# Performance work log

Hardware: AMD Instinct MI355X
Metric: run time of the kernel (lower is better)

## Reference

```python
import jax, jax.numpy as jnp
import jax.scipy.linalg as jsp
import numpy as np

# Problem dimensions (match init_kwargs P_shape/A_shape)
N = 256   # variables
M = 512   # constraints
B = 64    # batch

# OSQP ADMM hyper-parameters (fixed-rho variant of the OSQP algorithm)
SIGMA = 1e-6
RHO = 0.1
ALPHA = 1.6
N_ITERS = 500


def setup_inputs() -> dict:
    key = jax.random.key(0)
    kP, kq, kA, kc = jax.random.split(key, 4)
    # P is diagonal with strictly positive entries -> PSD (values are the nnz of P)
    P_val = jax.random.uniform(kP, (B, N), dtype=jnp.float32) + 0.1
    q_val = jax.random.normal(kq, (B, N), dtype=jnp.float32)
    # A is a dense pattern; values stored row-major as its nnz vector
    A_val = jax.random.normal(kA, (B, M * N), dtype=jnp.float32) / np.sqrt(N)
    # Feasible box: l <= u by construction
    center = jax.random.normal(kc, (B, M), dtype=jnp.float32)
    l_val = center - 1.0
    u_val = center + 1.0
    return {"P_val": P_val, "q_val": q_val, "A_val": A_val, "l_val": l_val, "u_val": u_val}


def _admm_qp(P_val, q_val, A_val, l_val, u_val):
    """Batched OSQP-style ADMM solve of min 1/2 x'Px + q'x  s.t. l <= Ax <= u.

    P is diagonal (nnz pattern = diag), A is dense (nnz pattern = full m x n).
    """
    A = A_val.reshape(B, M, N)                      # [B,m,n]
    # KKT-like matrix M_k = P + sigma*I + rho*A'A   [B,n,n]
    eye = jnp.eye(N, dtype=P_val.dtype)
    P_diag = P_val + SIGMA                          # diagonal of P + sigma*I
    Mk = RHO * jnp.einsum('bmi,bmj->bij', A, A) + jax.vmap(jnp.diag)(P_diag)
    L = jnp.linalg.cholesky(Mk)                     # [B,n,n], factor once, reuse
    Lt = jnp.swapaxes(L, -1, -2)

    def kkt_solve(rhs):                             # rhs [B,n]
        y1 = jsp.solve_triangular(L, rhs[..., None], lower=True)
        y2 = jsp.solve_triangular(Lt, y1, lower=False)
        return y2[..., 0]

    x0 = jnp.zeros((B, N), dtype=P_val.dtype)
    z0 = jnp.zeros((B, M), dtype=P_val.dtype)
    y0 = jnp.zeros((B, M), dtype=P_val.dtype)

    def step(state, _):
        x, z, y = state
        rhs = SIGMA * x - q_val + jnp.einsum('bmn,bm->bn', A, RHO * z - y)
        x_t = kkt_solve(rhs)                        # x-tilde
        z_t = jnp.einsum('bmn,bn->bm', A, x_t)      # z-tilde = A x_t
        x_new = ALPHA * x_t + (1.0 - ALPHA) * x
        z_hat = ALPHA * z_t + (1.0 - ALPHA) * z
        z_new = jnp.clip(z_hat + y / RHO, l_val, u_val)
        y_new = y + RHO * (z_hat - z_new)
        return (x_new, z_new, y_new), None

    (x, _, _), _ = jax.lax.scan(step, (x0, z0, y0), None, length=N_ITERS)
    return x


def reference(P_val, q_val, A_val, l_val, u_val):
    return _admm_qp(P_val, q_val, A_val, l_val, u_val)   # [B, n] primal solutions
```

## Files before the change

kernel.cpp:

```cpp
#include <hip/hip_runtime.h>
#include <hip/hip_fp16.h>

#define N_VAR 256
#define M_CON 512
#define BATCH 64
#define SIGMA_C 1e-6f
#define RHO_C 0.1f
#define ALPHA_C 1.6f
#define NITERS 500

__global__ __launch_bounds__(256) void k_transpose(const float* __restrict__ A,
                                                   float* __restrict__ At) {
  __shared__ float tile[32][33];
  int b = blockIdx.z;
  int n0 = blockIdx.x * 32;
  int m0 = blockIdx.y * 32;
  const float* Ab = A + (size_t)b * (M_CON * N_VAR);
  float* Atb = At + (size_t)b * (M_CON * N_VAR);
  int tx = threadIdx.x, ty = threadIdx.y;
#pragma unroll
  for (int j = 0; j < 32; j += 8)
    tile[ty + j][tx] = Ab[(size_t)(m0 + ty + j) * N_VAR + n0 + tx];
  __syncthreads();
#pragma unroll
  for (int j = 0; j < 32; j += 8)
    Atb[(size_t)(n0 + ty + j) * M_CON + m0 + tx] = tile[tx][ty + j];
}

__global__ __launch_bounds__(256) void k_ntgemm(
    const float* __restrict__ X, const float* __restrict__ Y,
    float* __restrict__ C, int I, int J, int K,
    long long bsX, long long bsY, long long bsC, float alpha,
    const float* __restrict__ diagv, int tilesJ, int packC) {
  int b = blockIdx.y;
  int ti = blockIdx.x / tilesJ, tj = blockIdx.x % tilesJ;
  int i0 = ti * 128, j0 = tj * 128;
  const float* Xb = X + (size_t)b * bsX;
  const float* Yb = Y + (size_t)b * bsY;
  float* Cb = C + (size_t)b * bsC;
  __shared__ float Xs[16][128];
  __shared__ float Ys[16][128];
  int tid = threadIdx.x;
  int tx = tid & 15, ty = tid >> 4;
  float acc[8][8];
#pragma unroll
  for (int r = 0; r < 8; ++r)
#pragma unroll
    for (int c = 0; c < 8; ++c) acc[r][c] = 0.0f;

  for (int kk = 0; kk < K; kk += 16) {
#pragma unroll
    for (int v = 0; v < 2; ++v) {
      int idx = v * 256 + tid;
      int row = idx >> 2;
      int k4 = (idx & 3) * 4;
      float4 gx = *(const float4*)(Xb + (size_t)(i0 + row) * K + kk + k4);
      Xs[k4 + 0][row] = gx.x; Xs[k4 + 1][row] = gx.y;
      Xs[k4 + 2][row] = gx.z; Xs[k4 + 3][row] = gx.w;
      float4 gy = *(const float4*)(Yb + (size_t)(j0 + row) * K + kk + k4);
      Ys[k4 + 0][row] = gy.x; Ys[k4 + 1][row] = gy.y;
      Ys[k4 + 2][row] = gy.z; Ys[k4 + 3][row] = gy.w;
    }
    __syncthreads();
#pragma unroll
    for (int k = 0; k < 16; ++k) {
      float xr[8], yr[8];
      *(float4*)&xr[0] = *(float4*)&Xs[k][ty * 8];
      *(float4*)&xr[4] = *(float4*)&Xs[k][ty * 8 + 4];
      *(float4*)&yr[0] = *(float4*)&Ys[k][tx * 8];
      *(float4*)&yr[4] = *(float4*)&Ys[k][tx * 8 + 4];
#pragma unroll
      for (int r = 0; r < 8; ++r)
#pragma unroll
        for (int c = 0; c < 8; ++c) acc[r][c] += xr[r] * yr[c];
    }
    __syncthreads();
  }
  if (packC) {
    unsigned* Cp = (unsigned*)Cb;
#pragma unroll
    for (int r = 0; r < 8; ++r) {
      int gi = i0 + ty * 8 + r;
      int sl = gi >> 7, rl = gi & 127;
      int rh = rl >> 6, ll = rl & 63;
#pragma unroll
      for (int c = 0; c < 8; c += 2) {
        int gj = j0 + tx * 8 + c;
        int cg = gj >> 7, j2 = (gj & 127) >> 1;
        int t2 = ((((cg << 1) | rh) << 6) | ll);
        __half2 hh = __floats2half2_rn(acc[r][c] * alpha, acc[r][c + 1] * alpha);
        Cp[(size_t)sl * 32768 + j2 * 512 + t2] = *(unsigned*)&hh;
      }
    }
    return;
  }
#pragma unroll
  for (int r = 0; r < 8; ++r) {
    int gi = i0 + ty * 8 + r;
#pragma unroll
    for (int c = 0; c < 8; ++c) {
      int gj = j0 + tx * 8 + c;
      float val = acc[r][c] * alpha;
      if (diagv != nullptr && gi == gj) val += diagv[(size_t)b * N_VAR + gi] + SIGMA_C;
      Cb[(size_t)gi * J + gj] = val;
    }
  }
}

__global__ __launch_bounds__(512, 2) void k_invert(const float* __restrict__ Mk,
                                                   float* __restrict__ Mi) {
  int b = blockIdx.x;
  const float* src = Mk + (size_t)b * 65536;
  float* dst = Mi + (size_t)b * 65536;
  int t = threadIdx.x;
  int c = t & 255, rh = t >> 8;

  float a[128];
#pragma unroll
  for (int j = 0; j < 128; ++j) a[j] = src[(size_t)(rh * 128 + j) * 256 + c];

  __shared__ float colPan[256][8];
  __shared__ float rowPan[2][8][260];
  __shared__ float PiSh[64];
  __shared__ float Rp[8][260];

  int rh_s = __builtin_amdgcn_readfirstlane(rh);
  int cw_s = __builtin_amdgcn_readfirstlane((t >> 6) & 3);

  if (rh == 0) {
#pragma unroll
    for (int j = 0; j < 8; ++j) rowPan[0][j][c] = a[j];
  }
  __syncthreads();

  for (int s = 0; s < 32; ++s) {
    int kb = s * 8;
    int cur = s & 1, nxt = cur ^ 1;
    int kh = kb >> 7, kj = kb & 127;
    int khn = (kb + 8) >> 7, kjn = (kb + 8) & 127;
    bool mycol = (c >= kb) && (c < kb + 8);

    if (cw_s == (kb >> 6)) {
      if (mycol) {
        int f = c - kb;
#pragma unroll
        for (int j = 0; j < 128; ++j) colPan[rh * 128 + j][f] = a[j];
      }
    }
    if (t < 64) {
      int e = t >> 3, f = t & 7;
      float p = rowPan[cur][e][kb + f];
#pragma unroll
      for (int k2 = 0; k2 < 8; ++k2) {
        float piv = __shfl(p, k2 * 8 + k2);
        float rv = __shfl(p, k2 * 8 + f);
        float cv = __shfl(p, e * 8 + k2);
        float pivinv = 1.0f / piv;
        float srv = rv * pivinv;
        float gen = p - cv * srv;
        p = gen;
        if (e == k2) p = srv;
        if (f == k2) p = -cv * pivinv;
        if (e == k2 && f == k2) p = pivinv;
      }
      PiSh[t] = p;
    }
    __syncthreads();

    float rpan[8];
#pragma unroll
    for (int f2 = 0; f2 < 8; ++f2) rpan[f2] = rowPan[cur][f2][c];
    float rp[8];
#pragma unroll
    for (int e = 0; e < 8; ++e) {
      float4 p0 = *(const float4*)&PiSh[e * 8];
      float4 p1 = *(const float4*)&PiSh[e * 8 + 4];
      rp[e] = p0.x * rpan[0] + p0.y * rpan[1] + p0.z * rpan[2] + p0.w * rpan[3] +
              p1.x * rpan[4] + p1.y * rpan[5] + p1.z * rpan[6] + p1.w * rpan[7];
    }
    if (cw_s == (kb >> 6)) {
      if (mycol) {
        int f = c - kb;
#pragma unroll
        for (int e = 0; e < 8; ++e) rp[e] = PiSh[e * 8 + f];
      }
    }
#pragma unroll
    for (int e = 0; e < 8; ++e) Rp[e][c] = rp[e];

    bool myhalfk = (rh_s == kh);
    bool stashw = (s != 31) && (rh_s == khn);
#pragma unroll
    for (int j = 0; j < 128; ++j) {
      float4 c0 = *(const float4*)&colPan[rh * 128 + j][0];
      float4 c1 = *(const float4*)&colPan[rh * 128 + j][4];
      float aold = a[j];
      float nv = aold -
                 (c0.x * rp[0] + c0.y * rp[1] + c0.z * rp[2] + c0.w * rp[3] +
                  c1.x * rp[4] + c1.y * rp[5] + c1.z * rp[6] + c1.w * rp[7]);
      if (mycol) nv -= aold;
      if (myhalfk && j >= kj && j < kj + 8)
        nv = Rp[j - kj][c];
      a[j] = nv;
      if (stashw && j >= kjn && j < kjn + 8)
        rowPan[nxt][j - kjn][c] = nv;
    }
    __syncthreads();
  }

#pragma unroll
  for (int j = 0; j < 128; ++j) dst[(size_t)(rh * 128 + j) * 256 + c] = a[j];
}

__global__ __launch_bounds__(256) void k_matvec_h(const float* __restrict__ Mi,
                                                  const float* __restrict__ q,
                                                  float* __restrict__ h) {
  int b = blockIdx.x, t = threadIdx.x;
  __shared__ float qs[256];
  qs[t] = q[(size_t)b * 256 + t];
  __syncthreads();
  const float* Mb = Mi + (size_t)b * 65536;
  float acc = 0.0f;
  for (int k = 0; k < 256; ++k) acc += Mb[(size_t)k * 256 + t] * qs[k];
  h[(size_t)b * 256 + t] = acc;
}

__global__ __launch_bounds__(512) void k_matvec_d(const float* __restrict__ At,
                                                  const float* __restrict__ h,
                                                  float* __restrict__ d) {
  int b = blockIdx.x, t = threadIdx.x;
  __shared__ float hs[256];
  if (t < 256) hs[t] = h[(size_t)b * 256 + t];
  __syncthreads();
  const float* Ab = At + (size_t)b * 131072;
  float acc = 0.0f;
  for (int n = 0; n < 256; ++n) acc += Ab[(size_t)n * 512 + t] * hs[n];
  d[(size_t)b * 512 + t] = acc;
}

__global__ __launch_bounds__(512) void k_admm4(
    const unsigned* __restrict__ Gpk_g, const float* __restrict__ dvec,
    const float* __restrict__ lv, const float* __restrict__ uv,
    unsigned long long* __restrict__ wtag, float* __restrict__ Sbuf) {
  int g = blockIdx.x;
  int b = (g & 7) + 8 * ((g >> 3) & 7);
  int s = g >> 6;
  int t = threadIdx.x;
  int l = t & 63, wv = t >> 6;
  int c0 = wv * 64;
  int cg = wv >> 1, hc = wv & 1;

  __shared__ __align__(16) float wbuf[8][64];
  __shared__ float part[2][8][128];

  const unsigned* gsrc =
      Gpk_g + (size_t)(b * 4 + s) * 32768 + (size_t)(hc * 32) * 512 + cg * 128 + l;

  float zreg = 0.0f, yreg = 0.0f, Sreg = 0.0f;
  float lreg = 0.0f, ureg = 0.0f, dreg = 0.0f;
  if (t < 128) {
    lreg = lv[(size_t)b * 512 + s * 128 + t];
    ureg = uv[(size_t)b * 512 + s * 128 + t];
    dreg = dvec[(size_t)b * 512 + s * 128 + t];
  }
  wbuf[wv][l] = 0.0f;

  unsigned long long* wt0 = wtag + (size_t)b * 512;
  unsigned long long* wt1 = wtag + 32768 + (size_t)b * 512;
  const float4* wq4 = (const float4*)(wbuf[wv]);

  for (int it = 0; it < NITERS; ++it) {
    if (it > 0) {
      unsigned long long* wp = (it & 1) ? wt1 : wt0;
      unsigned want = (unsigned)it;
      unsigned long long v = __hip_atomic_load(&wp[c0 + l], __ATOMIC_RELAXED,
                                               __HIP_MEMORY_SCOPE_AGENT);
      bool got = ((unsigned)(v >> 32) == want);
      while (!__all(got)) {
        if (!got) {
          unsigned long long v2 = __hip_atomic_load(
              &wp[c0 + l], __ATOMIC_RELAXED, __HIP_MEMORY_SCOPE_AGENT);
          if ((unsigned)(v2 >> 32) == want) { v = v2; got = true; }
        }
      }
      wbuf[wv][l] = __uint_as_float((unsigned)(v & 0xffffffffu));
    }

    float r0a = 0.f, r0b = 0.f, r1a = 0.f, r1b = 0.f;
#pragma unroll
    for (int j = 0; j < 8; ++j) {
      float4 wa = wq4[2 * j];
      float4 wc = wq4[2 * j + 1];
      unsigned a0 = gsrc[(4 * j + 0) * 512];
      unsigned a1 = gsrc[(4 * j + 1) * 512];
      unsigned a2 = gsrc[(4 * j + 2) * 512];
      unsigned a3 = gsrc[(4 * j + 3) * 512];
      unsigned b0 = gsrc[(4 * j + 0) * 512 + 64];
      unsigned b1 = gsrc[(4 * j + 1) * 512 + 64];
      unsigned b2 = gsrc[(4 * j + 2) * 512 + 64];
      unsigned b3 = gsrc[(4 * j + 3) * 512 + 64];
      float2 fa0 = __half22float2(*(__half2*)&a0);
      float2 fa1 = __half22float2(*(__half2*)&a1);
      float2 fa2 = __half22float2(*(__half2*)&a2);
      float2 fa3 = __half22float2(*(__half2*)&a3);
      float2 fb0 = __half22float2(*(__half2*)&b0);
      float2 fb1 = __half22float2(*(__half2*)&b1);
      float2 fb2 = __half22float2(*(__half2*)&b2);
      float2 fb3 = __half22float2(*(__half2*)&b3);
      r0a += fa0.x * wa.x + fa0.y * wa.y + fa1.x * wa.z + fa1.y * wa.w;
      r0b += fa2.x * wc.x + fa2.y * wc.y + fa3.x * wc.z + fa3.y * wc.w;
      r1a += fb0.x * wa.x + fb0.y * wa.y + fb1.x * wa.z + fb1.y * wa.w;
      r1b += fb2.x * wc.x + fb2.y * wc.y + fb3.x * wc.z + fb3.y * wc.w;
    }
    int pp = it & 1;
    part[pp][wv][l] = r0a + r0b;
    part[pp][wv][64 + l] = r1a + r1b;
    __syncthreads();

    if (t < 128) {
      float w_old = RHO_C * zreg - yreg;
      Sreg = w_old - 0.6f * Sreg;
      float p = part[pp][0][t] + part[pp][1][t] + part[pp][2][t] +
                part[pp][3][t] + part[pp][4][t] + part[pp][5][t] +
                part[pp][6][t] + part[pp][7][t];
      float zt = p - dreg;
      float zh = ALPHA_C * zt + (1.0f - ALPHA_C) * zreg;
      float zc = zh + yreg * (1.0f / RHO_C);
      zc = fminf(fmaxf(zc, lreg), ureg);
      yreg += RHO_C * (zh - zc);
      zreg = zc;
      if (it < NITERS - 1) {
        float wn = RHO_C * zreg - yreg;
        unsigned long long pk =
            ((unsigned long long)(unsigned)(it + 1) << 32) |
            (unsigned long long)__float_as_uint(wn);
        unsigned long long* wp = ((it + 1) & 1) ? wt1 : wt0;
        __hip_atomic_store(&wp[s * 128 + t], pk, __ATOMIC_RELAXED,
                           __HIP_MEMORY_SCOPE_AGENT);
      }
    }
  }

  if (t < 128) Sbuf[(size_t)b * 512 + s * 128 + t] = Sreg;
}

__global__ __launch_bounds__(256) void k_final(
    const float* __restrict__ A, const float* __restrict__ q,
    const float* __restrict__ Mi, const float* __restrict__ Sbuf,
    float* __restrict__ xout) {
  int b = blockIdx.x, t = threadIdx.x;
  __shared__ float Ssh[512];
  __shared__ float uu[256];
  for (int i = t; i < 512; i += 256) Ssh[i] = Sbuf[(size_t)b * 512 + i];
  __syncthreads();
  const float* Ab = A + (size_t)b * 131072;
  float acc = 0.0f;
  for (int m = 0; m < 512; ++m) acc += Ab[(size_t)m * 256 + t] * Ssh[m];
  uu[t] = ALPHA_C * acc - q[(size_t)b * 256 + t];
  __syncthreads();
  const float* Mb = Mi + (size_t)b * 65536;
  float x = 0.0f;
  for (int kk = 0; kk < 256; ++kk) x += Mb[(size_t)kk * 256 + t] * uu[kk];
  xout[(size_t)b * 256 + t] = x;
}

extern "C" void kernel_launch(void* const* d_in, const int* in_sizes, int n_in,
                              void* d_out, int out_size, void* d_ws, size_t ws_size,
                              hipStream_t stream) {
  (void)in_sizes; (void)n_in; (void)out_size; (void)ws_size;
  const float* P = (const float*)d_in[0];
  const float* q = (const float*)d_in[1];
  const float* Av = (const float*)d_in[2];
  const float* lv = (const float*)d_in[3];
  const float* uv = (const float*)d_in[4];
  float* xout = (float*)d_out;

  float* ws = (float*)d_ws;
  float* At = ws;
  float* F  = ws;
  float* Mi = ws + 8388608;
  float* Mk = ws + 12582912;
  float* Gp = ws + 12582912;
  float* hv = ws + 29360128;
  float* dv = ws + 29376512;
  float* Sbuf = ws + 29409280;
  unsigned long long* wtag = (unsigned long long*)ws;

  k_transpose<<<dim3(8, 16, 64), dim3(32, 8), 0, stream>>>(Av, At);
  k_ntgemm<<<dim3(4, 64), 256, 0, stream>>>(At, At, Mk, 256, 256, 512,
                                            131072LL, 131072LL, 65536LL,
                                            RHO_C, P, 2, 0);
  k_invert<<<64, 512, 0, stream>>>(Mk, Mi);
  k_matvec_h<<<64, 256, 0, stream>>>(Mi, q, hv);
  k_matvec_d<<<64, 512, 0, stream>>>(At, hv, dv);
  k_ntgemm<<<dim3(8, 64), 256, 0, stream>>>(Av, Mi, F, 512, 256, 256,
                                            131072LL, 65536LL, 131072LL,
                                            1.0f, nullptr, 2, 0);
  k_ntgemm<<<dim3(16, 64), 256, 0, stream>>>(F, Av, Gp, 512, 512, 256,
                                             131072LL, 131072LL, 131072LL,
                                             1.0f, nullptr, 4, 1);
  k_admm4<<<256, 512, 0, stream>>>((const unsigned*)Gp, dv, lv, uv, wtag, Sbuf);
  k_final<<<64, 256, 0, stream>>>(Av, q, Mi, Sbuf, xout);
}
```

Measured before the change: 1.541 ms.

## Keep G block resident in registers and double ADMM block threads

The persistent ADMM kernel now launches 1024 threads per block. Each thread preloads its 32 packed half2 entries of the G submatrix into registers once, instead of re-reading them from global memory on every iteration. The per-iteration matvec then runs from registers against the shared w vector, with each wave handling one row half for one column group. The risk is register pressure under launch_bounds(1024,4), which could cause spills, and a larger block that may make the per-iteration barrier and cross-block spin synchronisation more expensive.

```diff
diff --git a/kernel.cpp b/kernel.cpp
--- a/kernel.cpp
+++ b/kernel.cpp
@@ -238,7 +238,7 @@
   d[(size_t)b * 512 + t] = acc;
 }
 
-__global__ __launch_bounds__(512) void k_admm4(
+__global__ __launch_bounds__(1024, 4) void k_admm4(
     const unsigned* __restrict__ Gpk_g, const float* __restrict__ dvec,
     const float* __restrict__ lv, const float* __restrict__ uv,
     unsigned long long* __restrict__ wtag, float* __restrict__ Sbuf) {
@@ -247,15 +247,20 @@
   int s = g >> 6;
   int t = threadIdx.x;
   int l = t & 63, wv = t >> 6;
-  int c0 = wv * 64;
-  int cg = wv >> 1, hc = wv & 1;
-
-  __shared__ __align__(16) float wbuf[8][64];
+  int cg = wv & 7, rh = wv >> 3;
+  int c0 = cg * 64;
+
+  __shared__ __align__(16) float wbuf[16][64];
   __shared__ float part[2][8][128];
 
-  const unsigned* gsrc =
-      Gpk_g + (size_t)(b * 4 + s) * 32768 + (size_t)(hc * 32) * 512 + cg * 128 + l;
-
+  const unsigned* gsrc = Gpk_g + (size_t)(b * 4 + s) * 32768 +
+                         (size_t)((cg & 1) * 32) * 512 + (cg >> 1) * 128 +
+                         rh * 64 + l;
+  unsigned Gw[32];
+#pragma unroll
+  for (int k = 0; k < 32; ++k) Gw[k] = gsrc[(size_t)k * 512];
+
+  int row_local = rh * 64 + l;
   float zreg = 0.0f, yreg = 0.0f, Sreg = 0.0f;
   float lreg = 0.0f, ureg = 0.0f, dreg = 0.0f;
   if (t < 128) {
@@ -267,7 +272,7 @@
 
   unsigned long long* wt0 = wtag + (size_t)b * 512;
   unsigned long long* wt1 = wtag + 32768 + (size_t)b * 512;
-  const float4* wq4 = (const float4*)(wbuf[wv]);
+  const float* wrow = wbuf[wv];
 
   for (int it = 0; it < NITERS; ++it) {
     if (it > 0) {
@@ -286,35 +291,26 @@
       wbuf[wv][l] = __uint_as_float((unsigned)(v & 0xffffffffu));
     }
 
-    float r0a = 0.f, r0b = 0.f, r1a = 0.f, r1b = 0.f;
-#pragma unroll
-    for (int j = 0; j < 8; ++j) {
-      float4 wa = wq4[2 * j];
-      float4 wc = wq4[2 * j + 1];
-      unsigned a0 = gsrc[(4 * j + 0) * 512];
-      unsigned a1 = gsrc[(4 * j + 1) * 512];
-      unsigned a2 = gsrc[(4 * j + 2) * 512];
-      unsigned a3 = gsrc[(4 * j + 3) * 512];
-      unsigned b0 = gsrc[(4 * j + 0) * 512 + 64];
-      unsigned b1 = gsrc[(4 * j + 1) * 512 + 64];
-      unsigned b2 = gsrc[(4 * j + 2) * 512 + 64];
-      unsigned b3 = gsrc[(4 * j + 3) * 512 + 64];
-      float2 fa0 = __half22float2(*(__half2*)&a0);
-      float2 fa1 = __half22float2(*(__half2*)&a1);
-      float2 fa2 = __half22float2(*(__half2*)&a2);
-      float2 fa3 = __half22float2(*(__half2*)&a3);
-      float2 fb0 = __half22float2(*(__half2*)&b0);
-      float2 fb1 = __half22float2(*(__half2*)&b1);
-      float2 fb2 = __half22float2(*(__half2*)&b2);
-      float2 fb3 = __half22float2(*(__half2*)&b3);
-      r0a += fa0.x * wa.x + fa0.y * wa.y + fa1.x * wa.z + fa1.y * wa.w;
-      r0b += fa2.x * wc.x + fa2.y * wc.y + fa3.x * wc.z + fa3.y * wc.w;
-      r1a += fb0.x * wa.x + fb0.y * wa.y + fb1.x * wa.z + fb1.y * wa.w;
-      r1b += fb2.x * wc.x + fb2.y * wc.y + fb3.x * wc.z + fb3.y * wc.w;
+    float a0 = 0.f, a1 = 0.f, a2 = 0.f, a3 = 0.f;
+#pragma unroll
+    for (int k = 0; k < 32; k += 4) {
+      float4 w0 = *(const float4*)&wrow[2 * k];
+      float4 w1 = *(const float4*)&wrow[2 * k + 4];
+      __half2 h0 = *(__half2*)&Gw[k];
+      __half2 h1 = *(__half2*)&Gw[k + 1];
+      __half2 h2 = *(__half2*)&Gw[k + 2];
+      __half2 h3 = *(__half2*)&Gw[k + 3];
+      a0 = fmaf(__half2float(__low2half(h0)), w0.x, a0);
+      a1 = fmaf(__half2float(__high2half(h0)), w0.y, a1);
+      a2 = fmaf(__half2float(__low2half(h1)), w0.z, a2);
+      a3 = fmaf(__half2float(__high2half(h1)), w0.w, a3);
+      a0 = fmaf(__half2float(__low2half(h2)), w1.x, a0);
+      a1 = fmaf(__half2float(__high2half(h2)), w1.y, a1);
+      a2 = fmaf(__half2float(__low2half(h3)), w1.z, a2);
+      a3 = fmaf(__half2float(__high2half(h3)), w1.w, a3);
     }
     int pp = it & 1;
-    part[pp][wv][l] = r0a + r0b;
-    part[pp][wv][64 + l] = r1a + r1b;
+    part[pp][cg][row_local] = (a0 + a1) + (a2 + a3);
     __syncthreads();
 
     if (t < 128) {
@@ -399,6 +395,6 @@
   k_ntgemm<<<dim3(16, 64), 256, 0, stream>>>(F, Av, Gp, 512, 512, 256,
                                              131072LL, 131072LL, 131072LL,
                                              1.0f, nullptr, 4, 1);
-  k_admm4<<<256, 512, 0, stream>>>((const unsigned*)Gp, dv, lv, uv, wtag, Sbuf);
+  k_admm4<<<256, 1024, 0, stream>>>((const unsigned*)Gp, dv, lv, uv, wtag, Sbuf);
   k_final<<<64, 256, 0, stream>>>(Av, q, Mi, Sbuf, xout);
 }
```

After: 1.673 ms. +8.5%, slower.

## Compute G = F·Aᵀ with split-fp16 MFMA and prefetch G loads in ADMM loop

Applied to the files above, without the earlier changes.

Replaces the fp32 SIMT GEMM that builds the packed G matrix with an MFMA kernel. Each fp32 operand is split into a high fp16 part plus a scaled fp16 residual, and three MFMA products recover near-fp32 accuracy. A cast-split kernel is added for A, and the F GEMM now writes hi/lo fp16 halves directly. The ADMM loop now loads all G values for an iteration into registers before the spin-wait, so the loads overlap the synchronisation. wtag moves to its own region with an explicit memset. The cost is extra passes and workspace, higher register pressure in k_admm4, and some precision risk from the fp16 split.

```diff
diff --git a/kernel.cpp b/kernel.cpp
--- a/kernel.cpp
+++ b/kernel.cpp
@@ -8,6 +8,9 @@
 #define RHO_C 0.1f
 #define ALPHA_C 1.6f
 #define NITERS 500
+
+typedef _Float16 f16x8 __attribute__((ext_vector_type(8)));
+typedef float f32x4 __attribute__((ext_vector_type(4)));
 
 __global__ __launch_bounds__(256) void k_transpose(const float* __restrict__ A,
                                                    float* __restrict__ At) {
@@ -29,7 +32,7 @@
 
 __global__ __launch_bounds__(256) void k_ntgemm(
     const float* __restrict__ X, const float* __restrict__ Y,
-    float* __restrict__ C, int I, int J, int K,
+    float* __restrict__ C, float* __restrict__ C2, int I, int J, int K,
     long long bsX, long long bsY, long long bsC, float alpha,
     const float* __restrict__ diagv, int tilesJ, int packC) {
   int b = blockIdx.y;
@@ -37,7 +40,6 @@
   int i0 = ti * 128, j0 = tj * 128;
   const float* Xb = X + (size_t)b * bsX;
   const float* Yb = Y + (size_t)b * bsY;
-  float* Cb = C + (size_t)b * bsC;
   __shared__ float Xs[16][128];
   __shared__ float Ys[16][128];
   int tid = threadIdx.x;
@@ -76,24 +78,28 @@
     }
     __syncthreads();
   }
-  if (packC) {
-    unsigned* Cp = (unsigned*)Cb;
+  if (packC == 2) {
+    unsigned* Ch = (unsigned*)C + (size_t)b * 65536;
+    unsigned* Ce = (unsigned*)C2 + (size_t)b * 65536;
 #pragma unroll
     for (int r = 0; r < 8; ++r) {
       int gi = i0 + ty * 8 + r;
-      int sl = gi >> 7, rl = gi & 127;
-      int rh = rl >> 6, ll = rl & 63;
 #pragma unroll
       for (int c = 0; c < 8; c += 2) {
         int gj = j0 + tx * 8 + c;
-        int cg = gj >> 7, j2 = (gj & 127) >> 1;
-        int t2 = ((((cg << 1) | rh) << 6) | ll);
-        __half2 hh = __floats2half2_rn(acc[r][c] * alpha, acc[r][c + 1] * alpha);
-        Cp[(size_t)sl * 32768 + j2 * 512 + t2] = *(unsigned*)&hh;
+        float v0 = acc[r][c] * alpha, v1 = acc[r][c + 1] * alpha;
+        __half2 hh = __floats2half2_rn(v0, v1);
+        float2 fb = __half22float2(hh);
+        __half2 he = __floats2half2_rn((v0 - fb.x) * 256.0f,
+                                       (v1 - fb.y) * 256.0f);
+        int idx = gi * 128 + (gj >> 1);
+        Ch[idx] = *(unsigned*)&hh;
+        Ce[idx] = *(unsigned*)&he;
       }
     }
     return;
   }
+  float* Cb = C + (size_t)b * bsC;
 #pragma unroll
   for (int r = 0; r < 8; ++r) {
     int gi = i0 + ty * 8 + r;
@@ -105,6 +111,90 @@
       Cb[(size_t)gi * J + gj] = val;
     }
   }
+}
+
+__global__ __launch_bounds__(256) void k_cast_split(
+    const float* __restrict__ in, unsigned* __restrict__ oh,
+    unsigned* __restrict__ oe, int n4) {
+  int i = blockIdx.x * 256 + threadIdx.x;
+  if (i >= n4) return;
+  float4 v = ((const float4*)in)[i];
+  __half2 h01 = __floats2half2_rn(v.x, v.y);
+  __half2 h23 = __floats2half2_rn(v.z, v.w);
+  float2 f01 = __half22float2(h01);
+  float2 f23 = __half22float2(h23);
+  __half2 e01 = __floats2half2_rn((v.x - f01.x) * 256.0f, (v.y - f01.y) * 256.0f);
+  __half2 e23 = __floats2half2_rn((v.z - f23.x) * 256.0f, (v.w - f23.y) * 256.0f);
+  uint2 uh; uh.x = *(unsigned*)&h01; uh.y = *(unsigned*)&h23;
+  uint2 ue; ue.x = *(unsigned*)&e01; ue.y = *(unsigned*)&e23;
+  ((uint2*)oh)[i] = uh;
+  ((uint2*)oe)[i] = ue;
+}
+
+__global__ __launch_bounds__(256, 4) void k_mfma_g(
+    const _Float16* __restrict__ Fh, const _Float16* __restrict__ Fe,
+    const _Float16* __restrict__ Ah, const _Float16* __restrict__ Ae,
+    unsigned* __restrict__ Gp) {
+  int b = blockIdx.y;
+  int bx = blockIdx.x;
+  int t = threadIdx.x, l = t & 63, wv = t >> 6;
+  int i0 = (bx >> 2) * 32;
+  int j0 = (bx & 3) * 128 + wv * 32;
+  const _Float16* Fhb = Fh + (size_t)b * 131072;
+  const _Float16* Feb = Fe + (size_t)b * 131072;
+  const _Float16* Ahb = Ah + (size_t)b * 131072;
+  const _Float16* Aeb = Ae + (size_t)b * 131072;
+  unsigned* Gpb = Gp + (size_t)b * 131072;
+
+  int lr = l & 15, lk = (l >> 4) * 8;
+  f32x4 acc00 = {0,0,0,0}, acc01 = {0,0,0,0}, acc10 = {0,0,0,0}, acc11 = {0,0,0,0};
+  f32x4 ar00 = {0,0,0,0}, ar01 = {0,0,0,0}, ar10 = {0,0,0,0}, ar11 = {0,0,0,0};
+
+  for (int kk = 0; kk < 256; kk += 32) {
+    f16x8 af0 = *(const f16x8*)&Fhb[(size_t)(i0 + lr) * 256 + kk + lk];
+    f16x8 af1 = *(const f16x8*)&Fhb[(size_t)(i0 + 16 + lr) * 256 + kk + lk];
+    f16x8 ae0 = *(const f16x8*)&Feb[(size_t)(i0 + lr) * 256 + kk + lk];
+    f16x8 ae1 = *(const f16x8*)&Feb[(size_t)(i0 + 16 + lr) * 256 + kk + lk];
+    f16x8 bf0 = *(const f16x8*)&Ahb[(size_t)(j0 + lr) * 256 + kk + lk];
+    f16x8 bf1 = *(const f16x8*)&Ahb[(size_t)(j0 + 16 + lr) * 256 + kk + lk];
+    f16x8 be0 = *(const f16x8*)&Aeb[(size_t)(j0 + lr) * 256 + kk + lk];
+    f16x8 be1 = *(const f16x8*)&Aeb[(size_t)(j0 + 16 + lr) * 256 + kk + lk];
+    acc00 = __builtin_amdgcn_mfma_f32_16x16x32_f16(af0, bf0, acc00, 0, 0, 0);
+    acc01 = __builtin_amdgcn_mfma_f32_16x16x32_f16(af0, bf1, acc01, 0, 0, 0);
+    acc10 = __builtin_amdgcn_mfma_f32_16x16x32_f16(af1, bf0, acc10, 0, 0, 0);
+    acc11 = __builtin_amdgcn_mfma_f32_16x16x32_f16(af1, bf1, acc11, 0, 0, 0);
+    ar00 = __builtin_amdgcn_mfma_f32_16x16x32_f16(af0, be0, ar00, 0, 0, 0);
+    ar01 = __builtin_amdgcn_mfma_f32_16x16x32_f16(af0, be1, ar01, 0, 0, 0);
+    ar10 = __builtin_amdgcn_mfma_f32_16x16x32_f16(af1, be0, ar10, 0, 0, 0);
+    ar11 = __builtin_amdgcn_mfma_f32_16x16x32_f16(af1, be1, ar11, 0, 0, 0);
+    ar00 = __builtin_amdgcn_mfma_f32_16x16x32_f16(ae0, bf0, ar00, 0, 0, 0);
+    ar01 = __builtin_amdgcn_mfma_f32_16x16x32_f16(ae0, bf1, ar01, 0, 0, 0);
+    ar10 = __builtin_amdgcn_mfma_f32_16x16x32_f16(ae1, bf0, ar10, 0, 0, 0);
+    ar11 = __builtin_amdgcn_mfma_f32_16x16x32_f16(ae1, bf1, ar11, 0, 0, 0);
+  }
+
+#pragma unroll
+  for (int tr = 0; tr < 2; ++tr)
+#pragma unroll
+    for (int tc = 0; tc < 2; ++tc) {
+      const f32x4* am = (tr == 0) ? ((tc == 0) ? &acc00 : &acc01)
+                                  : ((tc == 0) ? &acc10 : &acc11);
+      const f32x4* ae = (tr == 0) ? ((tc == 0) ? &ar00 : &ar01)
+                                  : ((tc == 0) ? &ar10 : &ar11);
+#pragma unroll
+      for (int r = 0; r < 4; ++r) {
+        float v = (*am)[r] + (*ae)[r] * (1.0f / 256.0f);
+        float vp = __shfl_xor(v, 1);
+        int gi = i0 + tr * 16 + (l >> 4) * 4 + r;
+        int gj = j0 + tc * 16 + lr;
+        if (!(l & 1)) {
+          __half2 hh = __floats2half2_rn(v, vp);
+          int sl = gi >> 7, rl = gi & 127;
+          int t2 = ((((gj >> 7) << 1) | (rl >> 6)) << 6) | (rl & 63);
+          Gpb[(size_t)sl * 32768 + ((gj & 127) >> 1) * 512 + t2] = *(unsigned*)&hh;
+        }
+      }
+    }
 }
 
 __global__ __launch_bounds__(512, 2) void k_invert(const float* __restrict__ Mk,
@@ -270,6 +360,13 @@
   const float4* wq4 = (const float4*)(wbuf[wv]);
 
   for (int it = 0; it < NITERS; ++it) {
+    unsigned gva[32], gvb[32];
+#pragma unroll
+    for (int k = 0; k < 32; ++k) {
+      gva[k] = gsrc[(size_t)k * 512];
+      gvb[k] = gsrc[(size_t)k * 512 + 64];
+    }
+
     if (it > 0) {
       unsigned long long* wp = (it & 1) ? wt1 : wt0;
       unsigned want = (unsigned)it;
@@ -291,22 +388,14 @@
     for (int j = 0; j < 8; ++j) {
       float4 wa = wq4[2 * j];
       float4 wc = wq4[2 * j + 1];
-      unsigned a0 = gsrc[(4 * j + 0) * 512];
-      unsigned a1 = gsrc[(4 * j + 1) * 512];
-      unsigned a2 = gsrc[(4 * j + 2) * 512];
-      unsigned a3 = gsrc[(4 * j + 3) * 512];
-      unsigned b0 = gsrc[(4 * j + 0) * 512 + 64];
-      unsigned b1 = gsrc[(4 * j + 1) * 512 + 64];
-      unsigned b2 = gsrc[(4 * j + 2) * 512 + 64];
-      unsigned b3 = gsrc[(4 * j + 3) * 512 + 64];
-      float2 fa0 = __half22float2(*(__half2*)&a0);
-      float2 fa1 = __half22float2(*(__half2*)&a1);
-      float2 fa2 = __half22float2(*(__half2*)&a2);
-      float2 fa3 = __half22float2(*(__half2*)&a3);
-      float2 fb0 = __half22float2(*(__half2*)&b0);
-      float2 fb1 = __half22float2(*(__half2*)&b1);
-      float2 fb2 = __half22float2(*(__half2*)&b2);
-      float2 fb3 = __half22float2(*(__half2*)&b3);
+      float2 fa0 = __half22float2(*(__half2*)&gva[4 * j + 0]);
+      float2 fa1 = __half22float2(*(__half2*)&gva[4 * j + 1]);
+      float2 fa2 = __half22float2(*(__half2*)&gva[4 * j + 2]);
+      float2 fa3 = __half22float2(*(__half2*)&gva[4 * j + 3]);
+      float2 fb0 = __half22float2(*(__half2*)&gvb[4 * j + 0]);
+      float2 fb1 = __half22float2(*(__half2*)&gvb[4 * j + 1]);
+      float2 fb2 = __half22float2(*(__half2*)&gvb[4 * j + 2]);
+      float2 fb3 = __half22float2(*(__half2*)&gvb[4 * j + 3]);
       r0a += fa0.x * wa.x + fa0.y * wa.y + fa1.x * wa.z + fa1.y * wa.w;
       r0b += fa2.x * wc.x + fa2.y * wc.y + fa3.x * wc.z + fa3.y * wc.w;
       r1a += fb0.x * wa.x + fb0.y * wa.y + fb1.x * wa.z + fb1.y * wa.w;
@@ -377,28 +466,34 @@
 
   float* ws = (float*)d_ws;
   float* At = ws;
-  float* F  = ws;
+  unsigned* Ah = (unsigned*)ws;
+  unsigned* Ae = (unsigned*)(ws + 4194304);
   float* Mi = ws + 8388608;
   float* Mk = ws + 12582912;
   float* Gp = ws + 12582912;
+  float* Fh = ws + 20971520;
+  float* Fe = ws + 25165824;
   float* hv = ws + 29360128;
   float* dv = ws + 29376512;
   float* Sbuf = ws + 29409280;
-  unsigned long long* wtag = (unsigned long long*)ws;
+  unsigned long long* wtag = (unsigned long long*)(ws + 29442048);
+
+  hipMemsetAsync(wtag, 0, 131072 * 4, stream);
 
   k_transpose<<<dim3(8, 16, 64), dim3(32, 8), 0, stream>>>(Av, At);
-  k_ntgemm<<<dim3(4, 64), 256, 0, stream>>>(At, At, Mk, 256, 256, 512,
+  k_ntgemm<<<dim3(4, 64), 256, 0, stream>>>(At, At, Mk, nullptr, 256, 256, 512,
                                             131072LL, 131072LL, 65536LL,
                                             RHO_C, P, 2, 0);
   k_invert<<<64, 512, 0, stream>>>(Mk, Mi);
   k_matvec_h<<<64, 256, 0, stream>>>(Mi, q, hv);
   k_matvec_d<<<64, 512, 0, stream>>>(At, hv, dv);
-  k_ntgemm<<<dim3(8, 64), 256, 0, stream>>>(Av, Mi, F, 512, 256, 256,
-                                            131072LL, 65536LL, 131072LL,
-                                            1.0f, nullptr, 2, 0);
-  k_ntgemm<<<dim3(16, 64), 256, 0, stream>>>(F, Av, Gp, 512, 512, 256,
-                                             131072LL, 131072LL, 131072LL,
-                                             1.0f, nullptr, 4, 1);
+  k_cast_split<<<8192, 256, 0, stream>>>(Av, Ah, Ae, 2097152);
+  k_ntgemm<<<dim3(8, 64), 256, 0, stream>>>(Av, Mi, Fh, Fe, 512, 256, 256,
+                                            131072LL, 65536LL, 0LL,
+                                            1.0f, nullptr, 2, 2);
+  k_mfma_g<<<dim3(64, 64), 256, 0, stream>>>(
+      (const _Float16*)Fh, (const _Float16*)Fe,
+      (const _Float16*)Ah, (const _Float16*)Ae, (unsigned*)Gp);
   k_admm4<<<256, 512, 0, stream>>>((const unsigned*)Gp, dv, lv, uv, wtag, Sbuf);
   k_final<<<64, 256, 0, stream>>>(Av, q, Mi, Sbuf, xout);
 }
```

After: 1.539 ms. No clear change (-0.1%).
